# Performance work log

Hardware: AMD Instinct MI355X
Metric: run time of the kernel (lower is better)

The kernel has to match this reference:

```python
import jax, jax.numpy as jnp
import numpy as np

HIDDEN = 512
EPS = 1e-5  # BatchNorm1d default eps


def _ligru_layer(x, Ww, Wu, gamma, beta):
    # x: [T, B, F] time-major. Bidirectional: stack flipped copy along batch.
    x2 = jnp.concatenate([x, x[::-1]], axis=1)          # [T, 2B, F]
    w = jnp.einsum('tbf,gf->tbg', x2, Ww)               # [T, 2B, 2H]
    # BatchNorm over flattened (T*2B) rows, per feature (training-mode stats)
    mean = jnp.mean(w, axis=(0, 1))
    var = jnp.mean((w - mean) ** 2, axis=(0, 1))
    w = gamma * (w - mean) * jax.lax.rsqrt(var + EPS) + beta

    H = Wu.shape[1]
    h0 = jnp.zeros((w.shape[1], H), dtype=w.dtype)

    def step(h, wk):
        gates = wk + h @ Wu.T                            # [2B, 2H]
        at, zt = gates[:, :H], gates[:, H:]
        zt = jax.nn.sigmoid(zt)
        hcand = jax.nn.relu(at)                          # drop_mask == 1 (dropout=0)
        h = zt * h + (1.0 - zt) * hcand
        return h, h

    _, h = jax.lax.scan(step, h0, w)                     # [T, 2B, H]
    B = x.shape[1]
    h_f, h_b = h[:, :B], h[:, B:]
    return jnp.concatenate([h_f, h_b[::-1]], axis=2)     # [T, B, 2H]


def setup_inputs() -> dict:
    key = jax.random.key(0)
    ks = jax.random.split(key, 7)
    B, T, F, H = 16, 500, 240, HIDDEN
    x = jax.random.normal(ks[0], (B, T, F), dtype=jnp.float32)
    # layer 0: in=F, layer 1: in=2H (bidirectional output)
    Ww0 = jax.random.normal(ks[1], (2 * H, F), dtype=jnp.float32) / np.sqrt(F)
    Wu0 = jax.random.normal(ks[2], (2 * H, H), dtype=jnp.float32) / np.sqrt(H)
    Ww1 = jax.random.normal(ks[3], (2 * H, 2 * H), dtype=jnp.float32) / np.sqrt(2 * H)
    Wu1 = jax.random.normal(ks[4], (2 * H, H), dtype=jnp.float32) / np.sqrt(H)
    g0 = jnp.ones((2 * H,), jnp.float32)
    b0 = jnp.zeros((2 * H,), jnp.float32)
    g1 = jnp.ones((2 * H,), jnp.float32)
    b1 = jnp.zeros((2 * H,), jnp.float32)
    return {"x": x, "Ww0": Ww0, "Wu0": Wu0, "g0": g0, "b0": b0,
            "Ww1": Ww1, "Wu1": Wu1, "g1": g1, "b1": b1}


def reference(x, Ww0, Wu0, g0, b0, Ww1, Wu1, g1, b1):
    h = x.transpose(1, 0, 2)                             # [T, B, F]
    h = _ligru_layer(h, Ww0, Wu0, g0, b0)                # [T, B, 2H]
    h = _ligru_layer(h, Ww1, Wu1, g1, b1)                # [T, B, 2H]
    return h.transpose(1, 0, 2)                          # [B, T, 2H]
```

## Files before the change

kernel.cpp:

```cpp
#include <hip/hip_runtime.h>
#include <math.h>
#include <stdint.h>

#define TT 500
#define B2 32
#define FF 240
#define HH 512
#define G2 1024
#define MROWS (TT*B2)
#define REC_WGS 8
#define FLAG_STRIDE 16
#define FLAGS_PER_LAYER (TT*8*FLAG_STRIDE)

typedef __attribute__((ext_vector_type(8))) short bf16x8;
typedef __attribute__((ext_vector_type(4))) short bf16x4;
typedef __attribute__((ext_vector_type(4))) float f32x4;

typedef __attribute__((address_space(1))) const unsigned int GU32;
typedef __attribute__((address_space(3))) unsigned int LU32;

static __device__ __forceinline__ unsigned short f2bf(float f) {
    union { float f; unsigned u; } v; v.f = f;
    unsigned r = v.u + 0x7FFFu + ((v.u >> 16) & 1u);
    return (unsigned short)(r >> 16);
}

static __device__ __forceinline__ void gload_lds16(const void* g, void* l) {
    __builtin_amdgcn_global_load_lds((GU32*)g, (LU32*)l, 16, 0, 0);
}

__global__ void zero_cnt(unsigned int* cnt) {
    cnt[blockIdx.x * 256 + threadIdx.x] = 0u;
}

__global__ __launch_bounds__(256)
void cvt_a0(const float* __restrict__ x, unsigned short* __restrict__ A0)
{
    const int idx = blockIdx.x * 256 + threadIdx.x;
    const int m = idx >> 5;
    const int k = (idx & 31) * 8;
    const int t = m >> 5, b2 = m & 31;
    bf16x8 o = {0,0,0,0,0,0,0,0};
    if (k < FF) {
        const float* p = (b2 < 16)
            ? x + ((size_t)(b2 * TT + t)) * FF + k
            : x + ((size_t)((b2 - 16) * TT + (TT - 1 - t))) * FF + k;
        f32x4 a = *(const f32x4*)p;
        f32x4 b = *(const f32x4*)(p + 4);
        #pragma unroll
        for (int j = 0; j < 4; ++j) { o[j] = (short)f2bf(a[j]); o[4+j] = (short)f2bf(b[j]); }
    }
    *(bf16x8*)(A0 + (size_t)m * 256 + k) = o;
}

template<int Kin, int Kout>
__global__ __launch_bounds__(256)
void cvt_pad(const float* __restrict__ src, unsigned short* __restrict__ dst)
{
    const int idx = blockIdx.x * 256 + threadIdx.x;
    const int r = idx / (Kout / 8);
    const int k = (idx % (Kout / 8)) * 8;
    bf16x8 o = {0,0,0,0,0,0,0,0};
    if (k + 8 <= Kin) {
        f32x4 a = *(const f32x4*)(src + (size_t)r * Kin + k);
        f32x4 b = *(const f32x4*)(src + (size_t)r * Kin + k + 4);
        #pragma unroll
        for (int j = 0; j < 4; ++j) { o[j] = (short)f2bf(a[j]); o[4+j] = (short)f2bf(b[j]); }
    }
    *(bf16x8*)(dst + (size_t)r * Kout + k) = o;
}

template<int K>
__global__ __launch_bounds__(256, 2)
void mfma_gemm(const unsigned short* __restrict__ A,
               const unsigned short* __restrict__ B,
               float* __restrict__ C)
{
    __shared__ alignas(16) char As[16384];
    __shared__ alignas(16) char Bs[16384];
    const int tid = threadIdx.x;
    const int wv = tid >> 6, l = tid & 63, l15 = l & 15, lg = l >> 4;
    const int m0 = blockIdx.x * 128, n0 = blockIdx.y * 128;
    const int wr = wv >> 1, wc = wv & 1;
    f32x4 acc[4][4];
    #pragma unroll
    for (int i = 0; i < 4; ++i)
        #pragma unroll
        for (int j = 0; j < 4; ++j) acc[i][j] = (f32x4){0.f, 0.f, 0.f, 0.f};

    for (int ko = 0; ko < K; ko += 64) {
        #pragma unroll
        for (int i = 0; i < 4; ++i) {
            const int ch = tid + i * 256;
            const int row = ch >> 3, q = ch & 7;
            const int kb = (q * 16) ^ ((row & 7) << 4);
            gload_lds16(A + (size_t)(m0 + row) * K + ko + (kb >> 1), As + ch * 16);
            gload_lds16(B + (size_t)(n0 + row) * K + ko + (kb >> 1), Bs + ch * 16);
        }
        __syncthreads();
        #pragma unroll
        for (int ks = 0; ks < 2; ++ks) {
            bf16x8 af[4], bf[4];
            #pragma unroll
            for (int ib = 0; ib < 4; ++ib) {
                const int r = wr * 64 + ib * 16 + l15;
                const int sz = (r & 7) << 4;
                const int kb0 = ks * 64 + lg * 8;
                bf16x4 lo = *(const bf16x4*)(As + r * 128 + (kb0 ^ sz));
                bf16x4 hi = *(const bf16x4*)(As + r * 128 + ((kb0 + 32) ^ sz));
                bf16x8 f;
                f[0]=lo[0]; f[1]=lo[1]; f[2]=lo[2]; f[3]=lo[3];
                f[4]=hi[0]; f[5]=hi[1]; f[6]=hi[2]; f[7]=hi[3];
                af[ib] = f;
            }
            #pragma unroll
            for (int jb = 0; jb < 4; ++jb) {
                const int r = wc * 64 + jb * 16 + l15;
                const int sz = (r & 7) << 4;
                const int kb0 = ks * 64 + lg * 8;
                bf16x4 lo = *(const bf16x4*)(Bs + r * 128 + (kb0 ^ sz));
                bf16x4 hi = *(const bf16x4*)(Bs + r * 128 + ((kb0 + 32) ^ sz));
                bf16x8 f;
                f[0]=lo[0]; f[1]=lo[1]; f[2]=lo[2]; f[3]=lo[3];
                f[4]=hi[0]; f[5]=hi[1]; f[6]=hi[2]; f[7]=hi[3];
                bf[jb] = f;
            }
            #pragma unroll
            for (int ib = 0; ib < 4; ++ib)
                #pragma unroll
                for (int jb = 0; jb < 4; ++jb)
                    acc[ib][jb] = __builtin_amdgcn_mfma_f32_16x16x32_bf16(af[ib], bf[jb], acc[ib][jb], 0, 0, 0);
        }
        __syncthreads();
    }
    #pragma unroll
    for (int ib = 0; ib < 4; ++ib)
        #pragma unroll
        for (int jb = 0; jb < 4; ++jb)
            #pragma unroll
            for (int rr = 0; rr < 4; ++rr)
                C[(size_t)(m0 + wr * 64 + ib * 16 + lg * 4 + rr) * G2 +
                  (n0 + wc * 64 + jb * 16 + l15)] = acc[ib][jb][rr];
}

__global__ __launch_bounds__(256)
void stats_partial(const float* __restrict__ w, float* __restrict__ partS,
                   float* __restrict__ partQ)
{
    const int col = blockIdx.x * 256 + threadIdx.x;
    const int row0 = blockIdx.y * 128;
    float s = 0.f, q = 0.f;
    for (int r = 0; r < 128; ++r) {
        float v = w[(size_t)(row0 + r) * G2 + col];
        s += v; q += v * v;
    }
    partS[blockIdx.y * G2 + col] = s;
    partQ[blockIdx.y * G2 + col] = q;
}

__global__ __launch_bounds__(256)
void stats_final(const float* __restrict__ partS, const float* __restrict__ partQ,
                 const float* __restrict__ gamma, const float* __restrict__ beta,
                 float* __restrict__ scale, float* __restrict__ shift)
{
    const int col = blockIdx.x * 256 + threadIdx.x;
    float s = 0.f, q = 0.f;
    for (int i = 0; i < 125; ++i) { s += partS[i * G2 + col]; q += partQ[i * G2 + col]; }
    const float mean = s * (1.f / 16000.f);
    float var = q * (1.f / 16000.f) - mean * mean;
    var = fmaxf(var, 0.f);
    const float sc = gamma[col] * rsqrtf(var + 1e-5f);
    scale[col] = sc;
    shift[col] = beta[col] - mean * sc;
}

template<int LAYER>
__global__ __launch_bounds__(512, 2)
void rec_kernel(const float* __restrict__ w, const float* __restrict__ scale,
                const float* __restrict__ shift, const float* __restrict__ Wu,
                void* __restrict__ outp, unsigned short* __restrict__ hx,
                unsigned int* __restrict__ flags)
{
    __shared__ alignas(16) char hbuf[2][32768];

    const int g   = blockIdx.x;
    const int tid = threadIdx.x;
    const int wv  = tid >> 6;
    const int l   = tid & 63;
    const int c   = 4 * g + (wv >> 1);
    const int m   = wv & 1;
    const int l15 = l & 15;
    const int lg  = l >> 4;
    const int jcol = 16 * c + l15;

    bf16x8 bfa[16], bfz[16];
    {
        const float* pa = Wu + (size_t)jcol * HH;
        const float* pz = Wu + (size_t)(HH + jcol) * HH;
        #pragma unroll
        for (int ks = 0; ks < 16; ++ks) {
            f32x4 a0 = *(const f32x4*)(pa + ks * 32 + lg * 4);
            f32x4 a1 = *(const f32x4*)(pa + ks * 32 + lg * 4 + 16);
            f32x4 z0 = *(const f32x4*)(pz + ks * 32 + lg * 4);
            f32x4 z1 = *(const f32x4*)(pz + ks * 32 + lg * 4 + 16);
            bf16x8 fa, fz;
            #pragma unroll
            for (int j = 0; j < 4; ++j) {
                fa[j]     = (short)f2bf(a0[j]);
                fa[4 + j] = (short)f2bf(a1[j]);
                fz[j]     = (short)f2bf(z0[j]);
                fz[4 + j] = (short)f2bf(z1[j]);
            }
            bfa[ks] = fa; bfz[ks] = fz;
        }
    }
    const float scl_a = scale[jcol],      sh_a = shift[jcol];
    const float scl_z = scale[HH + jcol], sh_z = shift[HH + jcol];

    float hold[4] = {0.f, 0.f, 0.f, 0.f};

    for (int i = tid; i < 4096; i += 512) ((uint4*)hbuf)[i] = make_uint4(0, 0, 0, 0);
    __syncthreads();

    for (int t = 0; t < TT; ++t) {
        const int p = t & 1;

        float wa_[4], wz_[4];
        #pragma unroll
        for (int r = 0; r < 4; ++r) {
            const int b = m * 16 + lg * 4 + r;
            const float* wp = w + ((size_t)t * B2 + b) * G2 + jcol;
            wa_[r] = wp[0];
            wz_[r] = wp[HH];
        }

        if (t > 0) {
            {
                const unsigned int* fl = flags + (size_t)(t - 1) * 8 * FLAG_STRIDE;
                unsigned v = 1u;
                do {
                    if (l < 8)
                        v = __hip_atomic_load(fl + l * FLAG_STRIDE, __ATOMIC_RELAXED,
                                              __HIP_MEMORY_SCOPE_AGENT);
                    if (__any(v == 0u)) __builtin_amdgcn_s_sleep(1); else break;
                } while (true);
            }
            const unsigned long long* src =
                (const unsigned long long*)hx + (size_t)(p ^ 1) * 4096;
            const int row = tid >> 4, hc = tid & 15;
            char* db = hbuf[p] + row * 1024;
            const int swz2 = (row & 7) << 4;
            unsigned long long vv[7];
            #pragma unroll
            for (int i = 0; i < 7; ++i) {
                const int sw = i + (i >= g);
                vv[i] = __hip_atomic_load(src + sw * 512 + row * 16 + hc,
                                          __ATOMIC_RELAXED, __HIP_MEMORY_SCOPE_AGENT);
            }
            #pragma unroll
            for (int i = 0; i < 7; ++i) {
                const int sw = i + (i >= g);
                *(unsigned long long*)(db + ((sw * 128 + hc * 8) ^ swz2)) = vv[i];
            }
            __syncthreads();
        }

        f32x4 aacc = {0.f, 0.f, 0.f, 0.f};
        f32x4 zacc = {0.f, 0.f, 0.f, 0.f};
        const int arow = m * 16 + l15;
        const char* rbase = hbuf[p] + arow * 1024;
        const int swz = (arow & 7) << 4;
        #pragma unroll
        for (int ks = 0; ks < 16; ++ks) {
            const int off0 = ks * 64 + lg * 8;
            bf16x4 h0 = *(const bf16x4*)(rbase + (off0 ^ swz));
            bf16x4 h1 = *(const bf16x4*)(rbase + ((off0 + 32) ^ swz));
            bf16x8 af;
            af[0] = h0[0]; af[1] = h0[1]; af[2] = h0[2]; af[3] = h0[3];
            af[4] = h1[0]; af[5] = h1[1]; af[6] = h1[2]; af[7] = h1[3];
            aacc = __builtin_amdgcn_mfma_f32_16x16x32_bf16(af, bfa[ks], aacc, 0, 0, 0);
            zacc = __builtin_amdgcn_mfma_f32_16x16x32_bf16(af, bfz[ks], zacc, 0, 0, 0);
        }

        #pragma unroll
        for (int r = 0; r < 4; ++r) {
            const int b = m * 16 + lg * 4 + r;
            const float aval = scl_a * wa_[r] + sh_a + aacc[r];
            const float zval = scl_z * wz_[r] + sh_z + zacc[r];
            const float zt = 1.f / (1.f + __expf(-zval));
            const float hn = zt * hold[r] + (1.f - zt) * fmaxf(aval, 0.f);
            hold[r] = hn;
            const unsigned short hb = f2bf(hn);
            if (LAYER == 0) {
                unsigned short* A1 = (unsigned short*)outp;
                const int cc = jcol + (m == 0 ? 0 : HH);
                const int r1 = t * B2 + b;
                const int r2 = (TT - 1 - t) * B2 + (m == 0 ? b + 16 : b - 16);
                A1[(size_t)r1 * G2 + cc] = hb;
                A1[(size_t)r2 * G2 + cc] = hb;
            } else {
                float* po = (float*)outp;
                const int bb = (m == 0) ? b : b - 16;
                const int tt = (m == 0) ? t : (TT - 1 - t);
                po[((size_t)bb * TT + tt) * G2 + jcol + (m == 0 ? 0 : HH)] = hn;
            }
            if (t < TT - 1)
                *(unsigned short*)(hbuf[p ^ 1] + b * 1024 +
                                   ((jcol * 2) ^ ((b & 7) << 4))) = hb;
        }

        if (t < TT - 1) {
            __syncthreads();
            {
                const int row = tid >> 4, ch = tid & 15;
                const int swz2 = (row & 7) << 4;
                const unsigned long long v = *(const unsigned long long*)
                    (hbuf[p ^ 1] + row * 1024 + ((128 * g + ch * 8) ^ swz2));
                __hip_atomic_store((unsigned long long*)hx + (size_t)p * 4096 +
                                       g * 512 + row * 16 + ch,
                                   v, __ATOMIC_RELAXED, __HIP_MEMORY_SCOPE_AGENT);
            }
            __syncthreads();
            if (tid == 0)
                __hip_atomic_fetch_add(flags + ((size_t)t * 8 + g) * FLAG_STRIDE, 1u,
                                       __ATOMIC_RELAXED, __HIP_MEMORY_SCOPE_AGENT);
        }
    }
}

extern "C" void kernel_launch(void* const* d_in, const int* in_sizes, int n_in,
                              void* d_out, int out_size, void* d_ws, size_t ws_size,
                              hipStream_t stream)
{
    const float* x   = (const float*)d_in[0];
    const float* Ww0 = (const float*)d_in[1];
    const float* Wu0 = (const float*)d_in[2];
    const float* g0  = (const float*)d_in[3];
    const float* b0  = (const float*)d_in[4];
    const float* Ww1 = (const float*)d_in[5];
    const float* Wu1 = (const float*)d_in[6];
    const float* g1  = (const float*)d_in[7];
    const float* b1  = (const float*)d_in[8];
    float* out = (float*)d_out;

    float* w     = (float*)d_ws;
    float* scr0  = w + (size_t)MROWS * G2;
    float* scr1  = scr0 + (size_t)TT * B2 * HH;
    float* partS = scr1 + (size_t)TT * B2 * HH;
    float* partQ = partS + 125 * G2;
    float* scale = partQ + 125 * G2;
    float* shift = scale + G2;
    unsigned int* flags = (unsigned int*)(shift + G2);
    unsigned short* hx  = (unsigned short*)(flags + 2 * FLAGS_PER_LAYER);

    unsigned short* A0b = (unsigned short*)scr0;
    unsigned short* Wwb = (unsigned short*)(scr0 + 3 * 1024 * 1024);
    unsigned short* A1b = (unsigned short*)scr1;

    const size_t needed = ((size_t)MROWS * G2 + 2 * (size_t)TT * B2 * HH +
                           2 * 125 * G2 + 2 * G2) * 4 +
                          (size_t)2 * FLAGS_PER_LAYER * 4 + 2 * 16384 * 2;
    if (ws_size < needed) return;

    zero_cnt<<<2 * FLAGS_PER_LAYER / 256, 256, 0, stream>>>(flags);

    cvt_a0<<<2000, 256, 0, stream>>>(x, A0b);
    cvt_pad<240, 256><<<128, 256, 0, stream>>>(Ww0, Wwb);
    mfma_gemm<256><<<dim3(125, 8), 256, 0, stream>>>(A0b, Wwb, w);
    stats_partial<<<dim3(4, 125), 256, 0, stream>>>(w, partS, partQ);
    stats_final<<<4, 256, 0, stream>>>(partS, partQ, g0, b0, scale, shift);
    rec_kernel<0><<<REC_WGS, 512, 0, stream>>>(w, scale, shift, Wu0, A1b, hx, flags);

    cvt_pad<1024, 1024><<<512, 256, 0, stream>>>(Ww1, Wwb);
    mfma_gemm<1024><<<dim3(125, 8), 256, 0, stream>>>(A1b, Wwb, w);
    stats_partial<<<dim3(4, 125), 256, 0, stream>>>(w, partS, partQ);
    stats_final<<<4, 256, 0, stream>>>(partS, partQ, g1, b1, scale, shift);
    rec_kernel<1><<<REC_WGS, 512, 0, stream>>>(w, scale, shift, Wu1, out, hx,
                                               flags + FLAGS_PER_LAYER);
}
```

Before: 2.755 ms.

## Split recurrent workgroups by direction to shrink per-step cross-workgroup exchange

Each recurrent workgroup now handles one direction (16 batch rows) and a quarter of the hidden columns instead of all 32 rows and an eighth of the columns. Since forward and backward recurrences are independent, each workgroup waits on only 4 peer flags and gathers 3 peer slices per timestep instead of 7, halving LDS use. Per-layer hidden-state exchange buffers are separated. The aim is to cut per-step synchronisation and exchange latency, the dominant cost of this serial loop, at the cost of each workgroup storing more columns per step.

```diff
diff --git a/kernel.cpp b/kernel.cpp
--- a/kernel.cpp
+++ b/kernel.cpp
@@ -15,6 +15,7 @@
 typedef __attribute__((ext_vector_type(8))) short bf16x8;
 typedef __attribute__((ext_vector_type(4))) short bf16x4;
 typedef __attribute__((ext_vector_type(4))) float f32x4;
+typedef unsigned long long u64;
 
 typedef __attribute__((address_space(1))) const unsigned int GU32;
 typedef __attribute__((address_space(3))) unsigned int LU32;
@@ -178,20 +179,22 @@
 __global__ __launch_bounds__(512, 2)
 void rec_kernel(const float* __restrict__ w, const float* __restrict__ scale,
                 const float* __restrict__ shift, const float* __restrict__ Wu,
-                void* __restrict__ outp, unsigned short* __restrict__ hx,
+                void* __restrict__ outp, u64* __restrict__ hx,
                 unsigned int* __restrict__ flags)
 {
-    __shared__ alignas(16) char hbuf[2][32768];
+    __shared__ alignas(16) char hbuf[2][16384];
 
     const int g   = blockIdx.x;
+    const int d   = g >> 2;
+    const int q   = g & 3;
     const int tid = threadIdx.x;
     const int wv  = tid >> 6;
     const int l   = tid & 63;
-    const int c   = 4 * g + (wv >> 1);
-    const int m   = wv & 1;
     const int l15 = l & 15;
     const int lg  = l >> 4;
-    const int jcol = 16 * c + l15;
+    const int jcol = 128 * q + 16 * wv + l15;
+
+    u64* hx_d = hx + (size_t)d * 4096;
 
     bf16x8 bfa[16], bfz[16];
     {
@@ -219,8 +222,11 @@
 
     float hold[4] = {0.f, 0.f, 0.f, 0.f};
 
-    for (int i = tid; i < 4096; i += 512) ((uint4*)hbuf)[i] = make_uint4(0, 0, 0, 0);
+    for (int i = tid; i < 2048; i += 512) ((uint4*)hbuf)[i] = make_uint4(0, 0, 0, 0);
     __syncthreads();
+
+    const int grow = tid >> 5, guc = tid & 31;
+    const int gswz = (grow & 7) << 4;
 
     for (int t = 0; t < TT; ++t) {
         const int p = t & 1;
@@ -228,46 +234,44 @@
         float wa_[4], wz_[4];
         #pragma unroll
         for (int r = 0; r < 4; ++r) {
-            const int b = m * 16 + lg * 4 + r;
-            const float* wp = w + ((size_t)t * B2 + b) * G2 + jcol;
+            const int b2 = d * 16 + lg * 4 + r;
+            const float* wp = w + ((size_t)t * B2 + b2) * G2 + jcol;
             wa_[r] = wp[0];
             wz_[r] = wp[HH];
         }
 
         if (t > 0) {
             {
-                const unsigned int* fl = flags + (size_t)(t - 1) * 8 * FLAG_STRIDE;
+                const unsigned int* fl = flags +
+                    ((size_t)(t - 1) * 8 + d * 4) * FLAG_STRIDE;
                 unsigned v = 1u;
                 do {
-                    if (l < 8)
+                    if (l < 4)
                         v = __hip_atomic_load(fl + l * FLAG_STRIDE, __ATOMIC_RELAXED,
                                               __HIP_MEMORY_SCOPE_AGENT);
                     if (__any(v == 0u)) __builtin_amdgcn_s_sleep(1); else break;
                 } while (true);
             }
-            const unsigned long long* src =
-                (const unsigned long long*)hx + (size_t)(p ^ 1) * 4096;
-            const int row = tid >> 4, hc = tid & 15;
-            char* db = hbuf[p] + row * 1024;
-            const int swz2 = (row & 7) << 4;
-            unsigned long long vv[7];
-            #pragma unroll
-            for (int i = 0; i < 7; ++i) {
-                const int sw = i + (i >= g);
-                vv[i] = __hip_atomic_load(src + sw * 512 + row * 16 + hc,
+            const u64* src = hx_d + (size_t)(p ^ 1) * 2048;
+            u64 vv[3];
+            #pragma unroll
+            for (int i = 0; i < 3; ++i) {
+                const int sw = i + (i >= q);
+                vv[i] = __hip_atomic_load(src + sw * 512 + grow * 32 + guc,
                                           __ATOMIC_RELAXED, __HIP_MEMORY_SCOPE_AGENT);
             }
-            #pragma unroll
-            for (int i = 0; i < 7; ++i) {
-                const int sw = i + (i >= g);
-                *(unsigned long long*)(db + ((sw * 128 + hc * 8) ^ swz2)) = vv[i];
+            char* db = hbuf[p] + grow * 1024;
+            #pragma unroll
+            for (int i = 0; i < 3; ++i) {
+                const int sw = i + (i >= q);
+                *(u64*)(db + ((sw * 256 + guc * 8) ^ gswz)) = vv[i];
             }
             __syncthreads();
         }
 
         f32x4 aacc = {0.f, 0.f, 0.f, 0.f};
         f32x4 zacc = {0.f, 0.f, 0.f, 0.f};
-        const int arow = m * 16 + l15;
+        const int arow = l15;
         const char* rbase = hbuf[p] + arow * 1024;
         const int swz = (arow & 7) << 4;
         #pragma unroll
@@ -284,7 +288,8 @@
 
         #pragma unroll
         for (int r = 0; r < 4; ++r) {
-            const int b = m * 16 + lg * 4 + r;
+            const int b  = lg * 4 + r;
+            const int b2 = d * 16 + b;
             const float aval = scl_a * wa_[r] + sh_a + aacc[r];
             const float zval = scl_z * wz_[r] + sh_z + zacc[r];
             const float zt = 1.f / (1.f + __expf(-zval));
@@ -293,16 +298,16 @@
             const unsigned short hb = f2bf(hn);
             if (LAYER == 0) {
                 unsigned short* A1 = (unsigned short*)outp;
-                const int cc = jcol + (m == 0 ? 0 : HH);
-                const int r1 = t * B2 + b;
-                const int r2 = (TT - 1 - t) * B2 + (m == 0 ? b + 16 : b - 16);
+                const int cc = jcol + (d == 0 ? 0 : HH);
+                const int r1 = t * B2 + b2;
+                const int r2 = (TT - 1 - t) * B2 + (d == 0 ? b2 + 16 : b2 - 16);
                 A1[(size_t)r1 * G2 + cc] = hb;
                 A1[(size_t)r2 * G2 + cc] = hb;
             } else {
                 float* po = (float*)outp;
-                const int bb = (m == 0) ? b : b - 16;
-                const int tt = (m == 0) ? t : (TT - 1 - t);
-                po[((size_t)bb * TT + tt) * G2 + jcol + (m == 0 ? 0 : HH)] = hn;
+                const int bb = (d == 0) ? b2 : b2 - 16;
+                const int tt = (d == 0) ? t : (TT - 1 - t);
+                po[((size_t)bb * TT + tt) * G2 + jcol + (d == 0 ? 0 : HH)] = hn;
             }
             if (t < TT - 1)
                 *(unsigned short*)(hbuf[p ^ 1] + b * 1024 +
@@ -312,18 +317,15 @@
         if (t < TT - 1) {
             __syncthreads();
             {
-                const int row = tid >> 4, ch = tid & 15;
-                const int swz2 = (row & 7) << 4;
-                const unsigned long long v = *(const unsigned long long*)
-                    (hbuf[p ^ 1] + row * 1024 + ((128 * g + ch * 8) ^ swz2));
-                __hip_atomic_store((unsigned long long*)hx + (size_t)p * 4096 +
-                                       g * 512 + row * 16 + ch,
+                const u64 v = *(const u64*)(hbuf[p ^ 1] + grow * 1024 +
+                                            ((256 * q + guc * 8) ^ gswz));
+                __hip_atomic_store(hx_d + (size_t)p * 2048 + q * 512 + grow * 32 + guc,
                                    v, __ATOMIC_RELAXED, __HIP_MEMORY_SCOPE_AGENT);
             }
             __syncthreads();
             if (tid == 0)
-                __hip_atomic_fetch_add(flags + ((size_t)t * 8 + g) * FLAG_STRIDE, 1u,
-                                       __ATOMIC_RELAXED, __HIP_MEMORY_SCOPE_AGENT);
+                __hip_atomic_fetch_add(flags + ((size_t)t * 8 + d * 4 + q) * FLAG_STRIDE,
+                                       1u, __ATOMIC_RELAXED, __HIP_MEMORY_SCOPE_AGENT);
         }
     }
 }
@@ -351,7 +353,8 @@
     float* scale = partQ + 125 * G2;
     float* shift = scale + G2;
     unsigned int* flags = (unsigned int*)(shift + G2);
-    unsigned short* hx  = (unsigned short*)(flags + 2 * FLAGS_PER_LAYER);
+    u64* hx0 = (u64*)(flags + 2 * FLAGS_PER_LAYER);
+    u64* hx1 = hx0 + 8192;
 
     unsigned short* A0b = (unsigned short*)scr0;
     unsigned short* Wwb = (unsigned short*)(scr0 + 3 * 1024 * 1024);
@@ -359,7 +362,7 @@
 
     const size_t needed = ((size_t)MROWS * G2 + 2 * (size_t)TT * B2 * HH +
                            2 * 125 * G2 + 2 * G2) * 4 +
-                          (size_t)2 * FLAGS_PER_LAYER * 4 + 2 * 16384 * 2;
+                          (size_t)2 * FLAGS_PER_LAYER * 4 + 16384 * 8;
     if (ws_size < needed) return;
 
     zero_cnt<<<2 * FLAGS_PER_LAYER / 256, 256, 0, stream>>>(flags);
@@ -369,12 +372,12 @@
     mfma_gemm<256><<<dim3(125, 8), 256, 0, stream>>>(A0b, Wwb, w);
     stats_partial<<<dim3(4, 125), 256, 0, stream>>>(w, partS, partQ);
     stats_final<<<4, 256, 0, stream>>>(partS, partQ, g0, b0, scale, shift);
-    rec_kernel<0><<<REC_WGS, 512, 0, stream>>>(w, scale, shift, Wu0, A1b, hx, flags);
+    rec_kernel<0><<<REC_WGS, 512, 0, stream>>>(w, scale, shift, Wu0, A1b, hx0, flags);
 
     cvt_pad<1024, 1024><<<512, 256, 0, stream>>>(Ww1, Wwb);
     mfma_gemm<1024><<<dim3(125, 8), 256, 0, stream>>>(A1b, Wwb, w);
     stats_partial<<<dim3(4, 125), 256, 0, stream>>>(w, partS, partQ);
     stats_final<<<4, 256, 0, stream>>>(partS, partQ, g1, b1, scale, shift);
-    rec_kernel<1><<<REC_WGS, 512, 0, stream>>>(w, scale, shift, Wu1, out, hx,
+    rec_kernel<1><<<REC_WGS, 512, 0, stream>>>(w, scale, shift, Wu1, out, hx1,
                                                flags + FLAGS_PER_LAYER);
 }
```

Result: faster. 2.479 ms (-10.0%).
